# Performance work log

Hardware: AMD Instinct MI355X
Metric: run time of the kernel (lower is better)

The kernel has to match this reference:

```python
import jax, jax.numpy as jnp
import numpy as np

IMG_CENTER = 112.0  # init arg; normalize() is unused in forward
EPS = 1e-12


def setup_inputs() -> dict:
    key = jax.random.key(0)
    kp, kg, km = jax.random.split(key, 3)
    B, N, M = 8, 4096, 4096
    pred = jax.random.normal(kp, (B, N, 3), jnp.float32)
    gt = jax.random.normal(kg, (B, M, 3), jnp.float32)
    # near-identity extrinsics with z-translation 5 so the perspective divide is stable
    base = jnp.concatenate([jnp.eye(3, dtype=jnp.float32),
                            jnp.array([[0.0], [0.0], [5.0]], jnp.float32)], axis=1)  # [3,4]
    proMatrix = base[None, :, :] + 0.05 * jax.random.normal(km, (B, 3, 4), jnp.float32)
    return {"pred": pred, "gt": gt, "proMatrix": proMatrix}


def _project(x, P):
    # x: [B, n, 3], P: [B, 3, 4] -> [B, n, 2] image-plane coords
    B, n, _ = x.shape
    hom = jnp.concatenate([x, jnp.ones((B, n, 1), x.dtype)], axis=2)  # [B, n, 4]
    posed = jnp.einsum('bij,bnj->bni', P, hom)                         # [B, n, 3]
    return posed[..., :2] / posed[..., 2:3]


def _chamfer(a, b):
    # a: [B, N, 2], b: [B, M, 2]; L2-norm (not squared) bidirectional chamfer
    d2 = (jnp.sum(a * a, -1)[:, :, None]
          + jnp.sum(b * b, -1)[:, None, :]
          - 2.0 * jnp.einsum('bnd,bmd->bnm', a, b))  # [B, N, M]
    d = jnp.sqrt(jnp.maximum(d2, EPS))
    per_b = jnp.mean(jnp.min(d, axis=2), axis=1) + jnp.mean(jnp.min(d, axis=1), axis=1)
    return jnp.mean(per_b)


def reference(pred, gt, proMatrix):
    gt_plane = _project(gt, proMatrix)
    pred_plane = _project(pred, proMatrix)
    return _chamfer(gt_plane, pred_plane)
```

## Files before the change

### kernel.cpp

```cpp
#include <hip/hip_runtime.h>
#include <math.h>

#define NPTS 4096
#define NB 8
#define NQTOT (2*NB*NPTS)
#define EPSF 1e-12f
#define NCHUNK 16
#define CCH 256
#define QPT 8

typedef float f32x2 __attribute__((ext_vector_type(2)));

static __device__ __forceinline__ f32x2 pk_fma_bx(f32x2 a, f32x2 b, f32x2 c){
    f32x2 d;
    asm("v_pk_fma_f32 %0, %1, %2, %3 op_sel:[0,0,0] op_sel_hi:[1,0,0]"
        : "=v"(d) : "v"(a), "v"(b), "v"(c));
    return d;
}
static __device__ __forceinline__ f32x2 pk_fma_by(f32x2 a, f32x2 b, f32x2 c){
    f32x2 d;
    asm("v_pk_fma_f32 %0, %1, %2, %3 op_sel:[0,1,0] op_sel_hi:[1,1,1]"
        : "=v"(d) : "v"(a), "v"(b), "v"(c));
    return d;
}
static __device__ __forceinline__ float fmin3(float a, float b, float c){
    float d;
    asm("v_min3_f32 %0, %1, %2, %3" : "=v"(d) : "v"(a), "v"(b), "v"(c));
    return d;
}

static __device__ __forceinline__ void project_pt(const float* __restrict__ p3,
                                                  const float* __restrict__ Pb,
                                                  float& ix, float& iy){
    float x = p3[0], y = p3[1], z = p3[2];
    float px = fmaf(Pb[0],x, fmaf(Pb[1],y, fmaf(Pb[2],z,  Pb[3])));
    float py = fmaf(Pb[4],x, fmaf(Pb[5],y, fmaf(Pb[6],z,  Pb[7])));
    float pz = fmaf(Pb[8],x, fmaf(Pb[9],y, fmaf(Pb[10],z, Pb[11])));
    ix = px / pz;
    iy = py / pz;
}

__global__ __launch_bounds__(256) void chamfer_fused(
        const float* __restrict__ pred, const float* __restrict__ gt,
        const float* __restrict__ P, float* __restrict__ minpart){
    __shared__ float4 cand[CCH];
    int bid   = blockIdx.x;
    int chunk = bid & 15;
    int qhalf = (bid >> 4) & 1;
    int b     = (bid >> 5) & 7;
    int dir   = (bid >> 8) & 1;
    int t = threadIdx.x;

    const float* Pb   = P + b * 12;
    const float* qsrc = dir ? pred : gt;
    const float* csrc = dir ? gt : pred;

    {
        const float* p3 = csrc + (size_t)(b*NPTS + chunk*CCH + t) * 3;
        float cx, cy; project_pt(p3, Pb, cx, cy);
        cand[t] = make_float4(-2.0f*cx, -2.0f*cy, fmaf(cx,cx, cy*cy), 0.0f);
    }

    f32x2 axp[4], ayp[4];
    float a2[QPT];
    #pragma unroll
    for (int q = 0; q < QPT; ++q){
        int qi = qhalf*(QPT*256) + q*256 + t;
        const float* p3 = qsrc + (size_t)(b*NPTS + qi) * 3;
        float ix, iy; project_pt(p3, Pb, ix, iy);
        axp[q>>1][q&1] = ix;
        ayp[q>>1][q&1] = iy;
        a2[q] = fmaf(ix,ix, iy*iy);
    }
    float mn[QPT];
    #pragma unroll
    for (int q = 0; q < QPT; ++q) mn[q] = 3.4e38f;

    __syncthreads();

    #pragma unroll 4
    for (int ci = 0; ci < CCH; ci += 2){
        float4 cd0 = cand[ci];
        float4 cd1 = cand[ci+1];
        f32x2 c0lo = {cd0.x, cd0.y}, c0hi = {cd0.z, cd0.w};
        f32x2 c1lo = {cd1.x, cd1.y}, c1hi = {cd1.z, cd1.w};
        #pragma unroll
        for (int p = 0; p < 4; ++p){
            f32x2 t0 = pk_fma_bx(axp[p], c0lo, c0hi);
            t0 = pk_fma_by(ayp[p], c0lo, t0);
            f32x2 t1 = pk_fma_bx(axp[p], c1lo, c1hi);
            t1 = pk_fma_by(ayp[p], c1lo, t1);
            mn[2*p]   = fmin3(t0.x, t1.x, mn[2*p]);
            mn[2*p+1] = fmin3(t0.y, t1.y, mn[2*p+1]);
        }
    }

    int gq = dir*(NB*NPTS) + b*NPTS + qhalf*(QPT*256) + t;
    #pragma unroll
    for (int q = 0; q < QPT; ++q){
        minpart[(size_t)chunk*NQTOT + gq + q*256] = mn[q] + a2[q];
    }
}

__global__ __launch_bounds__(256) void reduce_min_sum(
        const float* __restrict__ minpart, float* __restrict__ partials){
    __shared__ float sm[256];
    int t = threadIdx.x;
    int i = blockIdx.x * 256 + t;
    float m0 = minpart[i];
    #pragma unroll
    for (int c = 1; c < NCHUNK; ++c) m0 = fminf(m0, minpart[(size_t)c*NQTOT + i]);
    float s = sqrtf(fmaxf(m0, EPSF));
    sm[t] = s; __syncthreads();
    #pragma unroll
    for (int o = 128; o > 0; o >>= 1){
        if (t < o) sm[t] += sm[t + o];
        __syncthreads();
    }
    if (t == 0) partials[blockIdx.x] = sm[0];
}

__global__ void reduce_final(const float* __restrict__ partials,
                             float* __restrict__ out){
    __shared__ float sm[256];
    int t = threadIdx.x;
    sm[t] = partials[t];
    __syncthreads();
    #pragma unroll
    for (int o = 128; o > 0; o >>= 1){
        if (t < o) sm[t] += sm[t + o];
        __syncthreads();
    }
    if (t == 0) out[0] = sm[0] * (1.0f / 32768.0f);
}

extern "C" void kernel_launch(void* const* d_in, const int* in_sizes, int n_in,
                              void* d_out, int out_size, void* d_ws, size_t ws_size,
                              hipStream_t stream) {
    const float* pred = (const float*)d_in[0];
    const float* gt   = (const float*)d_in[1];
    const float* P    = (const float*)d_in[2];
    float* out = (float*)d_out;

    float* minpart  = (float*)d_ws;
    float* partials = (float*)((char*)d_ws + (size_t)NCHUNK*NQTOT*4);

    chamfer_fused<<<512, 256, 0, stream>>>(pred, gt, P, minpart);
    reduce_min_sum<<<256, 256, 0, stream>>>(minpart, partials);
    reduce_final<<<1, 256, 0, stream>>>(partials, out);
}
```

Before: 27.99 us.

## Retile chamfer to 16 queries per thread and fuse final reduction via last-block atomic

Each thread now holds 16 query points against 128-candidate chunks, so the whole 4096-query batch is covered by one block and there are 32 candidate chunks. This raises register reuse per LDS candidate load but doubles the partial-min buffer traffic. The separate final reduction launch is removed: the reduce kernel uses an atomic counter, reset by the first kernel, so the last block sums the partials. This saves one kernel launch at the cost of atomics and more register pressure.

```diff
diff --git a/kernel.cpp b/kernel.cpp
--- a/kernel.cpp
+++ b/kernel.cpp
@@ -5,9 +5,9 @@
 #define NB 8
 #define NQTOT (2*NB*NPTS)
 #define EPSF 1e-12f
-#define NCHUNK 16
-#define CCH 256
-#define QPT 8
+#define NCHUNK 32
+#define CCH 128
+#define QPT 16
 
 typedef float f32x2 __attribute__((ext_vector_type(2)));
 
@@ -42,30 +42,32 @@
 
 __global__ __launch_bounds__(256) void chamfer_fused(
         const float* __restrict__ pred, const float* __restrict__ gt,
-        const float* __restrict__ P, float* __restrict__ minpart){
+        const float* __restrict__ P, float* __restrict__ minpart,
+        unsigned* __restrict__ counter){
     __shared__ float4 cand[CCH];
     int bid   = blockIdx.x;
-    int chunk = bid & 15;
-    int qhalf = (bid >> 4) & 1;
+    int chunk = bid & 31;
     int b     = (bid >> 5) & 7;
     int dir   = (bid >> 8) & 1;
     int t = threadIdx.x;
+
+    if (bid == 0 && t == 0) *counter = 0;
 
     const float* Pb   = P + b * 12;
     const float* qsrc = dir ? pred : gt;
     const float* csrc = dir ? gt : pred;
 
-    {
+    if (t < CCH){
         const float* p3 = csrc + (size_t)(b*NPTS + chunk*CCH + t) * 3;
         float cx, cy; project_pt(p3, Pb, cx, cy);
         cand[t] = make_float4(-2.0f*cx, -2.0f*cy, fmaf(cx,cx, cy*cy), 0.0f);
     }
 
-    f32x2 axp[4], ayp[4];
+    f32x2 axp[QPT/2], ayp[QPT/2];
     float a2[QPT];
     #pragma unroll
     for (int q = 0; q < QPT; ++q){
-        int qi = qhalf*(QPT*256) + q*256 + t;
+        int qi = q*256 + t;
         const float* p3 = qsrc + (size_t)(b*NPTS + qi) * 3;
         float ix, iy; project_pt(p3, Pb, ix, iy);
         axp[q>>1][q&1] = ix;
@@ -85,7 +87,7 @@
         f32x2 c0lo = {cd0.x, cd0.y}, c0hi = {cd0.z, cd0.w};
         f32x2 c1lo = {cd1.x, cd1.y}, c1hi = {cd1.z, cd1.w};
         #pragma unroll
-        for (int p = 0; p < 4; ++p){
+        for (int p = 0; p < QPT/2; ++p){
             f32x2 t0 = pk_fma_bx(axp[p], c0lo, c0hi);
             t0 = pk_fma_by(ayp[p], c0lo, t0);
             f32x2 t1 = pk_fma_bx(axp[p], c1lo, c1hi);
@@ -95,7 +97,7 @@
         }
     }
 
-    int gq = dir*(NB*NPTS) + b*NPTS + qhalf*(QPT*256) + t;
+    int gq = dir*(NB*NPTS) + b*NPTS + t;
     #pragma unroll
     for (int q = 0; q < QPT; ++q){
         minpart[(size_t)chunk*NQTOT + gq + q*256] = mn[q] + a2[q];
@@ -103,8 +105,10 @@
 }
 
 __global__ __launch_bounds__(256) void reduce_min_sum(
-        const float* __restrict__ minpart, float* __restrict__ partials){
+        const float* __restrict__ minpart, float* __restrict__ partials,
+        unsigned* __restrict__ counter, float* __restrict__ out){
     __shared__ float sm[256];
+    __shared__ int isLast;
     int t = threadIdx.x;
     int i = blockIdx.x * 256 + t;
     float m0 = minpart[i];
@@ -117,21 +121,25 @@
         if (t < o) sm[t] += sm[t + o];
         __syncthreads();
     }
-    if (t == 0) partials[blockIdx.x] = sm[0];
-}
-
-__global__ void reduce_final(const float* __restrict__ partials,
-                             float* __restrict__ out){
-    __shared__ float sm[256];
-    int t = threadIdx.x;
-    sm[t] = partials[t];
+    if (t == 0){
+        __hip_atomic_store(&partials[blockIdx.x], sm[0],
+                           __ATOMIC_RELEASE, __HIP_MEMORY_SCOPE_AGENT);
+        unsigned prev = __hip_atomic_fetch_add(counter, 1u,
+                           __ATOMIC_ACQ_REL, __HIP_MEMORY_SCOPE_AGENT);
+        isLast = (prev == 255u);
+    }
     __syncthreads();
-    #pragma unroll
-    for (int o = 128; o > 0; o >>= 1){
-        if (t < o) sm[t] += sm[t + o];
-        __syncthreads();
+    if (isLast){
+        float v = __hip_atomic_load(&partials[t],
+                      __ATOMIC_ACQUIRE, __HIP_MEMORY_SCOPE_AGENT);
+        sm[t] = v; __syncthreads();
+        #pragma unroll
+        for (int o = 128; o > 0; o >>= 1){
+            if (t < o) sm[t] += sm[t + o];
+            __syncthreads();
+        }
+        if (t == 0) out[0] = sm[0] * (1.0f / 32768.0f);
     }
-    if (t == 0) out[0] = sm[0] * (1.0f / 32768.0f);
 }
 
 extern "C" void kernel_launch(void* const* d_in, const int* in_sizes, int n_in,
@@ -142,10 +150,10 @@
     const float* P    = (const float*)d_in[2];
     float* out = (float*)d_out;
 
-    float* minpart  = (float*)d_ws;
-    float* partials = (float*)((char*)d_ws + (size_t)NCHUNK*NQTOT*4);
+    float*    minpart  = (float*)d_ws;
+    float*    partials = (float*)((char*)d_ws + (size_t)NCHUNK*NQTOT*4);
+    unsigned* counter  = (unsigned*)((char*)d_ws + (size_t)NCHUNK*NQTOT*4 + 4096);
 
-    chamfer_fused<<<512, 256, 0, stream>>>(pred, gt, P, minpart);
-    reduce_min_sum<<<256, 256, 0, stream>>>(minpart, partials);
-    reduce_final<<<1, 256, 0, stream>>>(partials, out);
+    chamfer_fused<<<512, 256, 0, stream>>>(pred, gt, P, minpart, counter);
+    reduce_min_sum<<<256, 256, 0, stream>>>(minpart, partials, counter, out);
 }
```

Measured after the change: 36.31 us. 29.7% more time.

## Fuse chunk-min and reductions into one kernel using last-block atomic counters

Applied to the files above, without the earlier changes.

Merges the three kernels into one. The last block to finish each query group, detected with an atomic counter, reduces that group's 16 chunk minima. The last group then reduces the 32 group partials into the output. The minpart layout is regrouped per query group so that block can read it with float4 loads. This removes two kernel launches and the gaps between them, at the cost of a memset launch, atomics, and a serial tail executed by a few blocks.

```diff
diff --git a/kernel.cpp b/kernel.cpp
--- a/kernel.cpp
+++ b/kernel.cpp
@@ -3,11 +3,12 @@
 
 #define NPTS 4096
 #define NB 8
-#define NQTOT (2*NB*NPTS)
 #define EPSF 1e-12f
-#define NCHUNK 16
 #define CCH 256
 #define QPT 8
+#define NCHUNK 16
+#define NGROUP 32
+#define GQ 2048
 
 typedef float f32x2 __attribute__((ext_vector_type(2)));
 
@@ -40,15 +41,20 @@
     iy = py / pz;
 }
 
-__global__ __launch_bounds__(256) void chamfer_fused(
+__global__ __launch_bounds__(256) void chamfer_mega(
         const float* __restrict__ pred, const float* __restrict__ gt,
-        const float* __restrict__ P, float* __restrict__ minpart){
+        const float* __restrict__ P, float* __restrict__ minpart,
+        unsigned* __restrict__ cnt, float* __restrict__ partials,
+        float* __restrict__ out){
     __shared__ float4 cand[CCH];
+    __shared__ float sm[256];
+    __shared__ int flag;
     int bid   = blockIdx.x;
     int chunk = bid & 15;
     int qhalf = (bid >> 4) & 1;
     int b     = (bid >> 5) & 7;
     int dir   = (bid >> 8) & 1;
+    int g     = bid >> 4;
     int t = threadIdx.x;
 
     const float* Pb   = P + b * 12;
@@ -61,11 +67,11 @@
         cand[t] = make_float4(-2.0f*cx, -2.0f*cy, fmaf(cx,cx, cy*cy), 0.0f);
     }
 
-    f32x2 axp[4], ayp[4];
+    f32x2 axp[QPT/2], ayp[QPT/2];
     float a2[QPT];
     #pragma unroll
     for (int q = 0; q < QPT; ++q){
-        int qi = qhalf*(QPT*256) + q*256 + t;
+        int qi = qhalf*GQ + q*256 + t;
         const float* p3 = qsrc + (size_t)(b*NPTS + qi) * 3;
         float ix, iy; project_pt(p3, Pb, ix, iy);
         axp[q>>1][q&1] = ix;
@@ -85,7 +91,7 @@
         f32x2 c0lo = {cd0.x, cd0.y}, c0hi = {cd0.z, cd0.w};
         f32x2 c1lo = {cd1.x, cd1.y}, c1hi = {cd1.z, cd1.w};
         #pragma unroll
-        for (int p = 0; p < 4; ++p){
+        for (int p = 0; p < QPT/2; ++p){
             f32x2 t0 = pk_fma_bx(axp[p], c0lo, c0hi);
             t0 = pk_fma_by(ayp[p], c0lo, t0);
             f32x2 t1 = pk_fma_bx(axp[p], c1lo, c1hi);
@@ -95,43 +101,67 @@
         }
     }
 
-    int gq = dir*(NB*NPTS) + b*NPTS + qhalf*(QPT*256) + t;
+    float* gp = minpart + (size_t)g * (NCHUNK*GQ);
     #pragma unroll
     for (int q = 0; q < QPT; ++q){
-        minpart[(size_t)chunk*NQTOT + gq + q*256] = mn[q] + a2[q];
+        gp[chunk*GQ + q*256 + t] = mn[q] + a2[q];
     }
-}
 
-__global__ __launch_bounds__(256) void reduce_min_sum(
-        const float* __restrict__ minpart, float* __restrict__ partials){
-    __shared__ float sm[256];
-    int t = threadIdx.x;
-    int i = blockIdx.x * 256 + t;
-    float m0 = minpart[i];
-    #pragma unroll
-    for (int c = 1; c < NCHUNK; ++c) m0 = fminf(m0, minpart[(size_t)c*NQTOT + i]);
-    float s = sqrtf(fmaxf(m0, EPSF));
-    sm[t] = s; __syncthreads();
-    #pragma unroll
-    for (int o = 128; o > 0; o >>= 1){
-        if (t < o) sm[t] += sm[t + o];
-        __syncthreads();
+    __syncthreads();
+    if (t == 0){
+        unsigned prev = __hip_atomic_fetch_add(&cnt[g], 1u,
+                            __ATOMIC_ACQ_REL, __HIP_MEMORY_SCOPE_AGENT);
+        flag = (prev == NCHUNK-1);
     }
-    if (t == 0) partials[blockIdx.x] = sm[0];
-}
+    __syncthreads();
+    if (!flag) return;
 
-__global__ void reduce_final(const float* __restrict__ partials,
-                             float* __restrict__ out){
-    __shared__ float sm[256];
-    int t = threadIdx.x;
-    sm[t] = partials[t];
+    {
+        const float* gq0 = gp + t*8;
+        float4 m0 = *(const float4*)(gq0);
+        float4 m1 = *(const float4*)(gq0 + 4);
+        #pragma unroll
+        for (int c = 1; c < NCHUNK; ++c){
+            float4 v0 = *(const float4*)(gq0 + c*GQ);
+            float4 v1 = *(const float4*)(gq0 + c*GQ + 4);
+            m0.x = fminf(m0.x, v0.x); m0.y = fminf(m0.y, v0.y);
+            m0.z = fminf(m0.z, v0.z); m0.w = fminf(m0.w, v0.w);
+            m1.x = fminf(m1.x, v1.x); m1.y = fminf(m1.y, v1.y);
+            m1.z = fminf(m1.z, v1.z); m1.w = fminf(m1.w, v1.w);
+        }
+        float s = sqrtf(fmaxf(m0.x, EPSF)) + sqrtf(fmaxf(m0.y, EPSF))
+                + sqrtf(fmaxf(m0.z, EPSF)) + sqrtf(fmaxf(m0.w, EPSF))
+                + sqrtf(fmaxf(m1.x, EPSF)) + sqrtf(fmaxf(m1.y, EPSF))
+                + sqrtf(fmaxf(m1.z, EPSF)) + sqrtf(fmaxf(m1.w, EPSF));
+        sm[t] = s;
+    }
     __syncthreads();
     #pragma unroll
     for (int o = 128; o > 0; o >>= 1){
         if (t < o) sm[t] += sm[t + o];
         __syncthreads();
     }
-    if (t == 0) out[0] = sm[0] * (1.0f / 32768.0f);
+    if (t == 0){
+        __hip_atomic_store(&partials[g], sm[0],
+                           __ATOMIC_RELEASE, __HIP_MEMORY_SCOPE_AGENT);
+        unsigned p2 = __hip_atomic_fetch_add(&cnt[NGROUP], 1u,
+                           __ATOMIC_ACQ_REL, __HIP_MEMORY_SCOPE_AGENT);
+        flag = (p2 == NGROUP-1);
+    }
+    __syncthreads();
+    if (!flag) return;
+
+    if (t < NGROUP){
+        sm[t] = __hip_atomic_load(&partials[t],
+                    __ATOMIC_ACQUIRE, __HIP_MEMORY_SCOPE_AGENT);
+    }
+    __syncthreads();
+    if (t == 0){
+        float s = 0.0f;
+        #pragma unroll
+        for (int i = 0; i < NGROUP; ++i) s += sm[i];
+        out[0] = s * (1.0f / 32768.0f);
+    }
 }
 
 extern "C" void kernel_launch(void* const* d_in, const int* in_sizes, int n_in,
@@ -142,10 +172,11 @@
     const float* P    = (const float*)d_in[2];
     float* out = (float*)d_out;
 
-    float* minpart  = (float*)d_ws;
-    float* partials = (float*)((char*)d_ws + (size_t)NCHUNK*NQTOT*4);
+    const size_t MINPART_BYTES = (size_t)NGROUP * NCHUNK * GQ * 4;
+    float*    minpart  = (float*)d_ws;
+    unsigned* cnt      = (unsigned*)((char*)d_ws + MINPART_BYTES);
+    float*    partials = (float*)((char*)d_ws + MINPART_BYTES + 256);
 
-    chamfer_fused<<<512, 256, 0, stream>>>(pred, gt, P, minpart);
-    reduce_min_sum<<<256, 256, 0, stream>>>(minpart, partials);
-    reduce_final<<<1, 256, 0, stream>>>(partials, out);
+    hipMemsetAsync(cnt, 0, 256, stream);
+    chamfer_mega<<<512, 256, 0, stream>>>(pred, gt, P, minpart, cnt, partials, out);
 }
```

Measured after the change: 43.97 us. 57.1% more time.
